# Kernel optimization log

Measured on AMD Instinct MI355X. Metric: run time of the kernel, lower is better.

## Reference

```python
import jax, jax.numpy as jnp
import numpy as np

N_NODES = 100000


def gcn_conv(x, src, dst, W, b, n_nodes):
    # PyG GCNConv: x' = D^{-1/2} (A + I) D^{-1/2} (x @ W) + b
    # src/dst already include self-loops.
    h = x @ W  # [N, out]
    deg = jax.ops.segment_sum(jnp.ones_like(src, dtype=x.dtype), dst,
                              num_segments=n_nodes)  # includes self-loops -> deg >= 1
    dinv = jax.lax.rsqrt(deg)
    norm = dinv[src] * dinv[dst]  # [E+N]
    msgs = h[src] * norm[:, None]  # [E+N, out]
    out = jax.ops.segment_sum(msgs, dst, num_segments=n_nodes)
    return out + b


def setup_inputs() -> dict:
    key = jax.random.key(0)
    k1, k2, k3, k4 = jax.random.split(key, 4)
    in_dim, hid_dim, out_dim = 64, 128, 64
    n_edges = 1_600_000
    x = jax.random.normal(k1, (N_NODES, in_dim), dtype=jnp.float32)
    edge_index = jax.random.randint(k2, (2, n_edges), 0, N_NODES, dtype=jnp.int64)
    # Glorot-ish init for weights
    W1 = jax.random.normal(k3, (in_dim, hid_dim), dtype=jnp.float32) * (1.0 / np.sqrt(in_dim))
    W2 = jax.random.normal(k4, (hid_dim, out_dim), dtype=jnp.float32) * (1.0 / np.sqrt(hid_dim))
    b1 = jnp.zeros((hid_dim,), dtype=jnp.float32)
    b2 = jnp.zeros((out_dim,), dtype=jnp.float32)
    return {"x": x, "edge_index": edge_index, "W1": W1, "b1": b1, "W2": W2, "b2": b2}


def reference(x, edge_index, W1, b1, W2, b2):
    n = x.shape[0]
    loops = jnp.arange(n, dtype=edge_index.dtype)
    src = jnp.concatenate([edge_index[0], loops])
    dst = jnp.concatenate([edge_index[1], loops])
    h = gcn_conv(x, src, dst, W1, b1, n)
    h = jax.nn.relu(h)
    out = gcn_conv(h, src, dst, W2, b2, n)
    return out
```

## Files before the change

kernel.cpp:

```cpp
#include <hip/hip_runtime.h>
#include <hip/hip_fp16.h>


#define DIM 64
#define NB 256
#define SPAN 391
#define BK_TILE 4096
#define BK_PER 16

typedef _Float16 f16x8 __attribute__((ext_vector_type(8)));
typedef float f32x4 __attribute__((ext_vector_type(4)));

__device__ __forceinline__ void atomAddF(float* p, float v) {
    unsafeAtomicAdd(p, v);
}

__device__ __forceinline__ void h8_add(const float4 v, float* acc) {
    const __half2* hp = (const __half2*)&v;
    #pragma unroll
    for (int i = 0; i < 4; ++i) {
        float2 t = __half22float2(hp[i]);
        acc[2 * i] += t.x;
        acc[2 * i + 1] += t.y;
    }
}
__device__ __forceinline__ float4 f8_to_h8(const float* f) {
    __half2 hh[4];
    hh[0] = __float22half2_rn(make_float2(f[0], f[1]));
    hh[1] = __float22half2_rn(make_float2(f[2], f[3]));
    hh[2] = __float22half2_rn(make_float2(f[4], f[5]));
    hh[3] = __float22half2_rn(make_float2(f[6], f[7]));
    return *(float4*)hh;
}

__device__ __forceinline__ void gather1(const float4* __restrict__ h4,
                                        const int* __restrict__ col,
                                        int e, int e1, int lane, float* accA, float* accB) {
    for (; e + 8 <= e1; e += 8) {
        int s0 = col[e], s1 = col[e + 1], s2 = col[e + 2], s3 = col[e + 3];
        int s4 = col[e + 4], s5 = col[e + 5], s6 = col[e + 6], s7 = col[e + 7];
        float4 v0 = h4[(long)s0 * 8 + lane];
        float4 v1 = h4[(long)s1 * 8 + lane];
        float4 v2 = h4[(long)s2 * 8 + lane];
        float4 v3 = h4[(long)s3 * 8 + lane];
        float4 v4 = h4[(long)s4 * 8 + lane];
        float4 v5 = h4[(long)s5 * 8 + lane];
        float4 v6 = h4[(long)s6 * 8 + lane];
        float4 v7 = h4[(long)s7 * 8 + lane];
        h8_add(v0, accA); h8_add(v1, accB);
        h8_add(v2, accA); h8_add(v3, accB);
        h8_add(v4, accA); h8_add(v5, accB);
        h8_add(v6, accA); h8_add(v7, accB);
    }
    for (; e + 2 <= e1; e += 2) {
        float4 v0 = h4[(long)col[e] * 8 + lane];
        float4 v1 = h4[(long)col[e + 1] * 8 + lane];
        h8_add(v0, accA); h8_add(v1, accB);
    }
    if (e < e1) h8_add(h4[(long)col[e] * 8 + lane], accA);
}

__global__ __launch_bounds__(256) void k_wconv(const float* __restrict__ W1,
                                               const float* __restrict__ W2,
                                               _Float16* __restrict__ W1t,
                                               _Float16* __restrict__ W2t,
                                               int* __restrict__ bcnt) {
    int idx = blockIdx.x * 256 + threadIdx.x;
    if (blockIdx.x == 0) bcnt[threadIdx.x] = 0;
    if (idx < 8192) {
        int n = idx >> 6, k = idx & 63;
        W1t[idx] = (_Float16)W1[k * 128 + n];
    } else if (idx < 16384) {
        int j = idx - 8192;
        int n = j >> 7, k = j & 127;
        W2t[j] = (_Float16)W2[k * 64 + n];
    }
}

__global__ __launch_bounds__(256) void k_hist256(const int* __restrict__ ei,
                                                 int* __restrict__ bucketCnt, int E) {
    __shared__ int h[NB];
    const int tid = threadIdx.x;
    h[tid] = 0;
    __syncthreads();
    const int base = blockIdx.x * BK_TILE;
    #pragma unroll
    for (int j = 0; j < BK_TILE; j += 256) {
        int e = base + j + tid;
        if (e < E) atomicAdd(&h[(unsigned)ei[E + e] / (unsigned)SPAN], 1);
    }
    __syncthreads();
    if (h[tid]) atomicAdd(&bucketCnt[tid], h[tid]);
}
__global__ __launch_bounds__(256) void k_scan_b(const int* __restrict__ bucketCnt,
                                                int* __restrict__ bucketBase,
                                                int* __restrict__ gcur) {
    __shared__ int s[NB];
    const int tid = threadIdx.x;
    int v = bucketCnt[tid];
    s[tid] = v;
    __syncthreads();
    for (int off = 1; off < NB; off <<= 1) {
        int t = (tid >= off) ? s[tid - off] : 0;
        __syncthreads();
        s[tid] += t;
        __syncthreads();
    }
    int ex = s[tid] - v;
    bucketBase[tid] = ex;
    gcur[tid] = ex;
    if (tid == NB - 1) bucketBase[NB] = s[NB - 1];
}

__global__ __launch_bounds__(256) void k_bucket(const int* __restrict__ ei,
                                                int* __restrict__ gcur,
                                                unsigned* __restrict__ pairs, int E) {
    __shared__ int scn[NB];
    __shared__ int run[NB];
    __shared__ int lbase[NB];
    __shared__ int gbase[NB];
    __shared__ unsigned stage[BK_TILE];
    __shared__ unsigned char bkt[BK_TILE];
    const int tid = threadIdx.x;
    const int base = blockIdx.x * BK_TILE;

    scn[tid] = 0;
    __syncthreads();

    unsigned pv[BK_PER];
    int bv[BK_PER];
    #pragma unroll
    for (int j = 0; j < BK_PER; ++j) {
        int e = base + j * 256 + tid;
        if (e < E) {
            unsigned s = (unsigned)ei[e];
            unsigned d = (unsigned)ei[E + e];
            int b = (int)(d / (unsigned)SPAN);
            bv[j] = b;
            pv[j] = (s << 9) | (d - (unsigned)b * SPAN);
            atomicAdd(&scn[b], 1);
        } else bv[j] = -1;
    }
    __syncthreads();
    int c = scn[tid];
    for (int off = 1; off < 256; off <<= 1) {
        int t = (tid >= off) ? scn[tid - off] : 0;
        __syncthreads();
        scn[tid] += t;
        __syncthreads();
    }
    int ex = scn[tid] - c;
    lbase[tid] = ex;
    run[tid] = ex;
    if (c > 0) gbase[tid] = atomicAdd(&gcur[tid], c);
    __syncthreads();

    #pragma unroll
    for (int j = 0; j < BK_PER; ++j) {
        if (bv[j] >= 0) {
            int p = atomicAdd(&run[bv[j]], 1);
            stage[p] = pv[j];
            bkt[p] = (unsigned char)bv[j];
        }
    }
    __syncthreads();

    int total = min(BK_TILE, E - base);
    for (int i = tid; i < total; i += 256) {
        int bb = bkt[i];
        pairs[gbase[bb] + (i - lbase[bb])] = stage[i];
    }
}

__global__ __launch_bounds__(256) void k_finish(const unsigned* __restrict__ pairs,
                                                const int* __restrict__ bucketBase,
                                                int* __restrict__ row_ptr,
                                                float* __restrict__ dinv,
                                                int* __restrict__ col,
                                                const float* __restrict__ x,
                                                __half* __restrict__ Y, int N) {
    __shared__ int lh[512];
    __shared__ int sa[512];
    __shared__ int sb[512];
    __shared__ int lcur[SPAN];
    const int tid = threadIdx.x;
    const int b = blockIdx.x;
    const int lo = b * SPAN;
    const int hi = min(lo + SPAN, N);
    const int nn = hi - lo;
    const int p0 = bucketBase[b];
    const int p1 = bucketBase[b + 1];

    for (int i = tid; i < 512; i += 256) lh[i] = 0;
    __syncthreads();
    for (int e = p0 + tid; e < p1; e += 256)
        atomicAdd(&lh[pairs[e] & 511u], 1);
    __syncthreads();
    int* cur = sa;
    int* nxt = sb;
    for (int i = tid; i < 512; i += 256) sa[i] = lh[i];
    __syncthreads();
    for (int off = 1; off < 512; off <<= 1) {
        for (int i = tid; i < 512; i += 256)
            nxt[i] = cur[i] + ((i >= off) ? cur[i - off] : 0);
        __syncthreads();
        int* t = cur; cur = nxt; nxt = t;
    }
    for (int i = tid; i < nn; i += 256) {
        int cnt  = lh[i];
        int base = p0 + cur[i] - cnt;
        row_ptr[lo + i] = base;
        lcur[i] = base;
        dinv[lo + i] = rsqrtf(1.0f + (float)cnt);
    }
    if (b == NB - 1 && tid == 0) row_ptr[N] = p1;
    __syncthreads();
    for (int e = p0 + tid; e < p1; e += 256) {
        unsigned pr = pairs[e];
        int pos = atomicAdd(&lcur[pr & 511u], 1);
        col[pos] = (int)(pr >> 9);
    }
    const int seg = tid & 7;
    for (int rr = tid >> 3; rr < nn; rr += 32) {
        float di = rsqrtf(1.0f + (float)lh[rr]);
        long row = lo + rr;
        float4 a = ((const float4*)x)[row * 16 + seg * 2];
        float4 c = ((const float4*)x)[row * 16 + seg * 2 + 1];
        float f[8] = {a.x * di, a.y * di, a.z * di, a.w * di,
                      c.x * di, c.y * di, c.z * di, c.w * di};
        ((float4*)Y)[row * 8 + seg] = f8_to_h8(f);
    }
}

__global__ __launch_bounds__(256) void k_agg_fin(const int* __restrict__ row_ptr,
                                                 const int* __restrict__ col,
                                                 const float* __restrict__ dinv,
                                                 const __half* __restrict__ ph,
                                                 const float* __restrict__ bias,
                                                 float* __restrict__ outv, int n) {
    int g = blockIdx.x * 32 + (threadIdx.x >> 3);
    if (g >= n) return;
    int lane = threadIdx.x & 7;
    const float4* h4 = (const float4*)ph;
    float accA[8] = {}, accB[8] = {};
    h8_add(h4[(long)g * 8 + lane], accA);
    gather1(h4, col, row_ptr[g], row_ptr[g + 1], lane, accA, accB);

    float di = dinv[g];
    float r[8];
    #pragma unroll
    for (int i = 0; i < 8; ++i) r[i] = (accA[i] + accB[i]) * di;
    float4 b0 = ((const float4*)bias)[lane * 2];
    float4 b1v = ((const float4*)bias)[lane * 2 + 1];
    r[0] += b0.x; r[1] += b0.y; r[2] += b0.z; r[3] += b0.w;
    r[4] += b1v.x; r[5] += b1v.y; r[6] += b1v.z; r[7] += b1v.w;
    *(float4*)&outv[(long)g * 64 + lane * 8]     = make_float4(r[0], r[1], r[2], r[3]);
    *(float4*)&outv[(long)g * 64 + lane * 8 + 4] = make_float4(r[4], r[5], r[6], r[7]);
}

__global__ __launch_bounds__(128) void k_agg_mlp(const int* __restrict__ row_ptr,
                                                 const int* __restrict__ col,
                                                 const float* __restrict__ dinv,
                                                 const __half* __restrict__ Y,
                                                 const _Float16* __restrict__ W1t,
                                                 const float* __restrict__ b1,
                                                 const _Float16* __restrict__ W2t,
                                                 _Float16* __restrict__ X,
                                                 int M) {
    __shared__ __align__(16) _Float16 Xs[32 * 72];
    __shared__ __align__(16) _Float16 Hs[32 * 136];
    const int tid = threadIdx.x;
    const int row0 = blockIdx.x * 32;
    const int grp = tid >> 3;
    const int lane = tid & 7;
    const float4* h4 = (const float4*)Y;

    #pragma unroll
    for (int hh = 0; hh < 2; ++hh) {
        const int lrow = grp + hh * 16;
        const int g = row0 + lrow;
        float r[8] = {};
        if (g < M) {
            float accA[8] = {}, accB[8] = {};
            h8_add(h4[(long)g * 8 + lane], accA);
            gather1(h4, col, row_ptr[g], row_ptr[g + 1], lane, accA, accB);
            float di = dinv[g];
            #pragma unroll
            for (int i = 0; i < 8; ++i) r[i] = (accA[i] + accB[i]) * di;
        }
        *(float4*)&Xs[lrow * 72 + lane * 8] = f8_to_h8(r);
    }
    __syncthreads();

    const int wv = tid >> 6;
    const int l64 = tid & 63;
    const int lr = l64 & 15;
    const int lg = l64 >> 4;

    f16x8 a0 = *(const f16x8*)&Xs[(wv * 16 + lr) * 72 + lg * 8];
    f16x8 a1 = *(const f16x8*)&Xs[(wv * 16 + lr) * 72 + 32 + lg * 8];
    const _Float16* wb1 = W1t + lr * 64 + lg * 8;
    f32x4 acc[8];
    #pragma unroll
    for (int nt = 0; nt < 8; ++nt) acc[nt] = (f32x4){0.f, 0.f, 0.f, 0.f};
    #pragma unroll
    for (int nt = 0; nt < 8; ++nt) {
        f16x8 b0 = *(const f16x8*)(wb1 + nt * 1024);
        f16x8 bK = *(const f16x8*)(wb1 + nt * 1024 + 32);
        acc[nt] = __builtin_amdgcn_mfma_f32_16x16x32_f16(a0, b0, acc[nt], 0, 0, 0);
        acc[nt] = __builtin_amdgcn_mfma_f32_16x16x32_f16(a1, bK, acc[nt], 0, 0, 0);
    }
    #pragma unroll
    for (int nt = 0; nt < 8; ++nt) {
        float bv = b1[nt * 16 + lr];
        #pragma unroll
        for (int r = 0; r < 4; ++r) {
            float h = fmaxf(acc[nt][r] + bv, 0.f);
            Hs[(wv * 16 + lg * 4 + r) * 136 + nt * 16 + lr] = (_Float16)h;
        }
    }
    __syncthreads();

    const _Float16* wb2 = W2t + lr * 128 + lg * 8;
    const _Float16* hrow = &Hs[(wv * 16 + lr) * 136 + lg * 8];
    f32x4 acc2[4];
    #pragma unroll
    for (int nt = 0; nt < 4; ++nt) acc2[nt] = (f32x4){0.f, 0.f, 0.f, 0.f};
    #pragma unroll
    for (int kk = 0; kk < 4; ++kk) {
        f16x8 a = *(const f16x8*)(hrow + kk * 32);
        #pragma unroll
        for (int nt = 0; nt < 4; ++nt) {
            f16x8 b = *(const f16x8*)(wb2 + nt * 2048 + kk * 32);
            acc2[nt] = __builtin_amdgcn_mfma_f32_16x16x32_f16(a, b, acc2[nt], 0, 0, 0);
        }
    }
    _Float16* Os = Xs;
    float sc[4];
    #pragma unroll
    for (int r = 0; r < 4; ++r) {
        int gr = row0 + wv * 16 + lg * 4 + r;
        sc[r] = (gr < M) ? dinv[gr] : 0.f;
    }
    #pragma unroll
    for (int nt = 0; nt < 4; ++nt) {
        #pragma unroll
        for (int r = 0; r < 4; ++r)
            Os[(wv * 16 + lg * 4 + r) * 72 + nt * 16 + lr] = (_Float16)(acc2[nt][r] * sc[r]);
    }
    __syncthreads();

    {
        int r = tid >> 2, c0 = (tid & 3) * 16;
        int gr = row0 + r;
        if (gr < M) {
            f16x8 v0 = *(const f16x8*)&Os[r * 72 + c0];
            f16x8 v1 = *(const f16x8*)&Os[r * 72 + c0 + 8];
            *(f16x8*)(X + (long)gr * 64 + c0) = v0;
            *(f16x8*)(X + (long)gr * 64 + c0 + 8) = v1;
        }
    }
}

__global__ __launch_bounds__(256) void k_init_deg(float* deg, int n) {
    int i = blockIdx.x * 256 + threadIdx.x;
    if (i < n) deg[i] = 1.0f;
}
__global__ __launch_bounds__(256) void k_count_deg(const int* __restrict__ ei, float* deg, int E) {
    int e = blockIdx.x * 256 + threadIdx.x;
    if (e < E) atomAddF(&deg[ei[E + e]], 1.0f);
}
__global__ __launch_bounds__(256) void k_rsqrt(float* deg, int n) {
    int i = blockIdx.x * 256 + threadIdx.x;
    if (i < n) deg[i] = rsqrtf(deg[i]);
}
template<bool BIAS>
__global__ __launch_bounds__(256) void k_self(const float* __restrict__ src,
                                              const float* __restrict__ dinv,
                                              const float* __restrict__ b,
                                              float* __restrict__ out, int n) {
    int g = blockIdx.x * 256 + threadIdx.x;
    int i = g >> 4, c = g & 15;
    if (i >= n) return;
    float di = dinv[i];
    float s = di * di;
    float4 v = *(const float4*)&src[(long)i * DIM + c * 4];
    float4 r = make_float4(v.x * s, v.y * s, v.z * s, v.w * s);
    if (BIAS) {
        float4 bv = *(const float4*)&b[c * 4];
        r.x += bv.x; r.y += bv.y; r.z += bv.z; r.w += bv.w;
    }
    *(float4*)&out[(long)i * DIM + c * 4] = r;
}
__global__ __launch_bounds__(256) void k_edge_agg(const int* __restrict__ ei,
                                                  const float* __restrict__ dinv,
                                                  const float* __restrict__ h,
                                                  float* __restrict__ out, int E) {
    int t = threadIdx.x;
    int e = blockIdx.x * 16 + (t >> 4);
    if (e >= E) return;
    int lane = t & 15;
    int s = ei[e];
    int d = ei[E + e];
    float norm = dinv[s] * dinv[d];
    float4 hv = *(const float4*)&h[(long)s * DIM + lane * 4];
    float* o = &out[(long)d * DIM + lane * 4];
    atomAddF(o + 0, hv.x * norm);
    atomAddF(o + 1, hv.y * norm);
    atomAddF(o + 2, hv.z * norm);
    atomAddF(o + 3, hv.w * norm);
}
__global__ __launch_bounds__(256) void k_mlp_f(const float* __restrict__ G,
                                               const float* __restrict__ W1,
                                               const float* __restrict__ b1,
                                               const float* __restrict__ W2,
                                               float* __restrict__ T, int M) {
    __shared__ float Ws[64 * 128];
    __shared__ float HA[64 * 132];
    const int tid = threadIdx.x;
    const int row0 = blockIdx.x * 64;
    const int ty = tid >> 4;
    const int tx = tid & 15;
    #pragma unroll
    for (int l = 0; l < 4; ++l) {
        int idx = l * 256 + tid;
        int r = idx >> 4, cv = idx & 15;
        int gr = row0 + r;
        float4 v = make_float4(0.f, 0.f, 0.f, 0.f);
        if (gr < M) v = *(const float4*)&G[(long)gr * DIM + cv * 4];
        *(float4*)&HA[r * 68 + cv * 4] = v;
    }
    #pragma unroll
    for (int l = 0; l < 8; ++l) {
        int idx = (l * 256 + tid) * 4;
        *(float4*)&Ws[idx] = *(const float4*)&W1[idx];
    }
    __syncthreads();
    float4 accA[4], accB[4];
    #pragma unroll
    for (int i = 0; i < 4; ++i) {
        accA[i] = make_float4(0.f, 0.f, 0.f, 0.f);
        accB[i] = make_float4(0.f, 0.f, 0.f, 0.f);
    }
    for (int k4 = 0; k4 < 64; k4 += 4) {
        float4 a[4];
        #pragma unroll
        for (int i = 0; i < 4; ++i) a[i] = *(const float4*)&HA[(ty * 4 + i) * 68 + k4];
        #pragma unroll
        for (int kk = 0; kk < 4; ++kk) {
            const float* wr = &Ws[(k4 + kk) * 128 + tx * 8];
            float4 wA = *(const float4*)wr;
            float4 wB = *(const float4*)(wr + 4);
            #pragma unroll
            for (int i = 0; i < 4; ++i) {
                float ak = (&a[i].x)[kk];
                accA[i].x += ak * wA.x; accA[i].y += ak * wA.y;
                accA[i].z += ak * wA.z; accA[i].w += ak * wA.w;
                accB[i].x += ak * wB.x; accB[i].y += ak * wB.y;
                accB[i].z += ak * wB.z; accB[i].w += ak * wB.w;
            }
        }
    }
    __syncthreads();
    {
        float4 bA = *(const float4*)&b1[tx * 8];
        float4 bB = *(const float4*)&b1[tx * 8 + 4];
        #pragma unroll
        for (int i = 0; i < 4; ++i) {
            float4 hA = make_float4(fmaxf(accA[i].x + bA.x, 0.f), fmaxf(accA[i].y + bA.y, 0.f),
                                    fmaxf(accA[i].z + bA.z, 0.f), fmaxf(accA[i].w + bA.w, 0.f));
            float4 hB = make_float4(fmaxf(accB[i].x + bB.x, 0.f), fmaxf(accB[i].y + bB.y, 0.f),
                                    fmaxf(accB[i].z + bB.z, 0.f), fmaxf(accB[i].w + bB.w, 0.f));
            *(float4*)&HA[(ty * 4 + i) * 132 + tx * 8 + 0] = hA;
            *(float4*)&HA[(ty * 4 + i) * 132 + tx * 8 + 4] = hB;
        }
    }
    #pragma unroll
    for (int l = 0; l < 8; ++l) {
        int idx = (l * 256 + tid) * 4;
        *(float4*)&Ws[idx] = *(const float4*)&W2[idx];
    }
    __syncthreads();
    float4 o[4];
    #pragma unroll
    for (int i = 0; i < 4; ++i) o[i] = make_float4(0.f, 0.f, 0.f, 0.f);
    for (int k4 = 0; k4 < 128; k4 += 4) {
        float4 a[4];
        #pragma unroll
        for (int i = 0; i < 4; ++i) a[i] = *(const float4*)&HA[(ty * 4 + i) * 132 + k4];
        #pragma unroll
        for (int kk = 0; kk < 4; ++kk) {
            float4 w = *(const float4*)&Ws[(k4 + kk) * 64 + tx * 4];
            #pragma unroll
            for (int i = 0; i < 4; ++i) {
                float ak = (&a[i].x)[kk];
                o[i].x += ak * w.x; o[i].y += ak * w.y;
                o[i].z += ak * w.z; o[i].w += ak * w.w;
            }
        }
    }
    #pragma unroll
    for (int i = 0; i < 4; ++i) {
        int gr = row0 + ty * 4 + i;
        if (gr < M) *(float4*)&T[(long)gr * DIM + tx * 4] = o[i];
    }
}

extern "C" void kernel_launch(void* const* d_in, const int* in_sizes, int n_in,
                              void* d_out, int out_size, void* d_ws, size_t ws_size,
                              hipStream_t stream) {
    const float* x  = (const float*)d_in[0];
    const int*   ei = (const int*)d_in[1];
    const float* W1 = (const float*)d_in[2];
    const float* b1 = (const float*)d_in[3];
    const float* W2 = (const float*)d_in[4];
    const float* b2 = (const float*)d_in[5];
    float* out = (float*)d_out;

    const int N = in_sizes[0] / DIM;
    const int E = in_sizes[1] / 2;

    const int gn   = (N + 255) / 256;
    const int ge   = (E + 255) / 256;
    const int gagg = (N + 31) / 32;
    const int gmlp = (N + 63) / 64;
    const int gbk  = (E + BK_TILE - 1) / BK_TILE;

    size_t off = 0;
    auto bump = [&](size_t bytes) { size_t o = off; off = (off + bytes + 255) & ~(size_t)255; return o; };
    size_t o_dinv   = bump((size_t)N * 4);
    size_t o_rowptr = bump((size_t)(N + 1) * 4);
    size_t o_bcnt   = bump(NB * 4);
    size_t o_bbase  = bump((NB + 1) * 4);
    size_t o_gcur   = bump(NB * 4);
    size_t o_col    = bump((size_t)E * 4);
    size_t o_X      = bump((size_t)N * DIM * 2);
    size_t o_Y      = bump((size_t)N * DIM * 2);
    size_t o_pairs  = bump((size_t)E * 4);
    size_t o_W1t    = bump(128 * 64 * 2);
    size_t o_W2t    = bump(64 * 128 * 2);
    size_t need_csr = off;

    char* ws = (char*)d_ws;

    if (ws_size >= need_csr) {
        float*    dinv   = (float*)(ws + o_dinv);
        int*      rowptr = (int*)(ws + o_rowptr);
        int*      bcnt   = (int*)(ws + o_bcnt);
        int*      bbase  = (int*)(ws + o_bbase);
        int*      gcur   = (int*)(ws + o_gcur);
        int*      col    = (int*)(ws + o_col);
        __half*   X      = (__half*)(ws + o_X);
        __half*   Y      = (__half*)(ws + o_Y);
        unsigned* pairs  = (unsigned*)(ws + o_pairs);
        _Float16* W1t    = (_Float16*)(ws + o_W1t);
        _Float16* W2t    = (_Float16*)(ws + o_W2t);

        k_wconv<<<64, 256, 0, stream>>>(W1, W2, W1t, W2t, bcnt);
        k_hist256<<<gbk, 256, 0, stream>>>(ei, bcnt, E);
        k_scan_b<<<1, 256, 0, stream>>>(bcnt, bbase, gcur);
        k_bucket<<<gbk, 256, 0, stream>>>(ei, gcur, pairs, E);
        k_finish<<<NB, 256, 0, stream>>>(pairs, bbase, rowptr, dinv, col, x, Y, N);
        k_agg_mlp<<<gagg, 128, 0, stream>>>(rowptr, col, dinv, Y, W1t, b1, W2t,
                                            (_Float16*)X, N);
        k_agg_fin<<<gagg, 256, 0, stream>>>(rowptr, col, dinv, X, b2, out, N);
    } else {
        float* dinv = (float*)ws;
        float* buf  = (float*)(ws + 512 * 1024);
        int grow16 = ((long)N * 16 + 255) / 256;
        int gedge = (E + 15) / 16;

        k_init_deg<<<gn, 256, 0, stream>>>(dinv, N);
        k_count_deg<<<ge, 256, 0, stream>>>(ei, dinv, E);
        k_rsqrt<<<gn, 256, 0, stream>>>(dinv, N);

        k_self<false><<<grow16, 256, 0, stream>>>(x, dinv, nullptr, buf, N);
        k_edge_agg<<<gedge, 256, 0, stream>>>(ei, dinv, x, buf, E);
        k_mlp_f<<<gmlp, 256, 0, stream>>>(buf, W1, b1, W2, buf, N);
        k_self<true><<<grow16, 256, 0, stream>>>(buf, dinv, b2, out, N);
        k_edge_agg<<<gedge, 256, 0, stream>>>(ei, dinv, buf, out, E);
    }
}
```

Measured before the change: 234.5 us.

## Split feature gathers into 16-column channel slabs for cache-resident aggregation

Measured after the change: 310.9 us. 1.33x slower.

```diff
diff --git a/kernel.cpp b/kernel.cpp
--- a/kernel.cpp
+++ b/kernel.cpp
@@ -33,31 +33,31 @@
     return *(float4*)hh;
 }
 
-__device__ __forceinline__ void gather1(const float4* __restrict__ h4,
+__device__ __forceinline__ void gatherc(const float4* __restrict__ P2,
                                         const int* __restrict__ col,
-                                        int e, int e1, int lane, float* accA, float* accB) {
+                                        int e, int e1, int p, float* accA, float* accB) {
     for (; e + 8 <= e1; e += 8) {
         int s0 = col[e], s1 = col[e + 1], s2 = col[e + 2], s3 = col[e + 3];
         int s4 = col[e + 4], s5 = col[e + 5], s6 = col[e + 6], s7 = col[e + 7];
-        float4 v0 = h4[(long)s0 * 8 + lane];
-        float4 v1 = h4[(long)s1 * 8 + lane];
-        float4 v2 = h4[(long)s2 * 8 + lane];
-        float4 v3 = h4[(long)s3 * 8 + lane];
-        float4 v4 = h4[(long)s4 * 8 + lane];
-        float4 v5 = h4[(long)s5 * 8 + lane];
-        float4 v6 = h4[(long)s6 * 8 + lane];
-        float4 v7 = h4[(long)s7 * 8 + lane];
+        float4 v0 = P2[(long)s0 * 2 + p];
+        float4 v1 = P2[(long)s1 * 2 + p];
+        float4 v2 = P2[(long)s2 * 2 + p];
+        float4 v3 = P2[(long)s3 * 2 + p];
+        float4 v4 = P2[(long)s4 * 2 + p];
+        float4 v5 = P2[(long)s5 * 2 + p];
+        float4 v6 = P2[(long)s6 * 2 + p];
+        float4 v7 = P2[(long)s7 * 2 + p];
         h8_add(v0, accA); h8_add(v1, accB);
         h8_add(v2, accA); h8_add(v3, accB);
         h8_add(v4, accA); h8_add(v5, accB);
         h8_add(v6, accA); h8_add(v7, accB);
     }
     for (; e + 2 <= e1; e += 2) {
-        float4 v0 = h4[(long)col[e] * 8 + lane];
-        float4 v1 = h4[(long)col[e + 1] * 8 + lane];
+        float4 v0 = P2[(long)col[e] * 2 + p];
+        float4 v1 = P2[(long)col[e + 1] * 2 + p];
         h8_add(v0, accA); h8_add(v1, accB);
     }
-    if (e < e1) h8_add(h4[(long)col[e] * 8 + lane], accA);
+    if (e < e1) h8_add(P2[(long)col[e] * 2 + p], accA);
 }
 
 __global__ __launch_bounds__(256) void k_wconv(const float* __restrict__ W1,
@@ -228,77 +228,66 @@
         float4 c = ((const float4*)x)[row * 16 + seg * 2 + 1];
         float f[8] = {a.x * di, a.y * di, a.z * di, a.w * di,
                       c.x * di, c.y * di, c.z * di, c.w * di};
-        ((float4*)Y)[row * 8 + seg] = f8_to_h8(f);
-    }
-}
-
-__global__ __launch_bounds__(256) void k_agg_fin(const int* __restrict__ row_ptr,
-                                                 const int* __restrict__ col,
-                                                 const float* __restrict__ dinv,
-                                                 const __half* __restrict__ ph,
-                                                 const float* __restrict__ bias,
-                                                 float* __restrict__ outv, int n) {
-    int g = blockIdx.x * 32 + (threadIdx.x >> 3);
+        __half* dst = Y + ((size_t)(seg >> 1) * N + row) * 16 + (seg & 1) * 8;
+        *(float4*)dst = f8_to_h8(f);
+    }
+}
+
+template<bool FINAL>
+__global__ __launch_bounds__(256) void k_aggc(const int* __restrict__ row_ptr,
+                                              const int* __restrict__ col,
+                                              const float* __restrict__ dinv,
+                                              const __half* __restrict__ slab,
+                                              const float* __restrict__ bias,
+                                              void* __restrict__ outv,
+                                              int c, int n) {
+    int g = blockIdx.x * 128 + (threadIdx.x >> 1);
     if (g >= n) return;
-    int lane = threadIdx.x & 7;
-    const float4* h4 = (const float4*)ph;
+    int p = threadIdx.x & 1;
+    const float4* P2 = (const float4*)slab;
     float accA[8] = {}, accB[8] = {};
-    h8_add(h4[(long)g * 8 + lane], accA);
-    gather1(h4, col, row_ptr[g], row_ptr[g + 1], lane, accA, accB);
+    h8_add(P2[(long)g * 2 + p], accA);
+    gatherc(P2, col, row_ptr[g], row_ptr[g + 1], p, accA, accB);
 
     float di = dinv[g];
     float r[8];
     #pragma unroll
     for (int i = 0; i < 8; ++i) r[i] = (accA[i] + accB[i]) * di;
-    float4 b0 = ((const float4*)bias)[lane * 2];
-    float4 b1v = ((const float4*)bias)[lane * 2 + 1];
-    r[0] += b0.x; r[1] += b0.y; r[2] += b0.z; r[3] += b0.w;
-    r[4] += b1v.x; r[5] += b1v.y; r[6] += b1v.z; r[7] += b1v.w;
-    *(float4*)&outv[(long)g * 64 + lane * 8]     = make_float4(r[0], r[1], r[2], r[3]);
-    *(float4*)&outv[(long)g * 64 + lane * 8 + 4] = make_float4(r[4], r[5], r[6], r[7]);
-}
-
-__global__ __launch_bounds__(128) void k_agg_mlp(const int* __restrict__ row_ptr,
-                                                 const int* __restrict__ col,
-                                                 const float* __restrict__ dinv,
-                                                 const __half* __restrict__ Y,
-                                                 const _Float16* __restrict__ W1t,
-                                                 const float* __restrict__ b1,
-                                                 const _Float16* __restrict__ W2t,
-                                                 _Float16* __restrict__ X,
-                                                 int M) {
-    __shared__ __align__(16) _Float16 Xs[32 * 72];
-    __shared__ __align__(16) _Float16 Hs[32 * 136];
+    if (FINAL) {
+        const float* bc = bias + c * 16 + p * 8;
+        #pragma unroll
+        for (int i = 0; i < 8; ++i) r[i] += bc[i];
+        float* o = (float*)outv + (long)g * 64 + c * 16 + p * 8;
+        *(float4*)o       = make_float4(r[0], r[1], r[2], r[3]);
+        *(float4*)(o + 4) = make_float4(r[4], r[5], r[6], r[7]);
+    } else {
+        __half* o = (__half*)outv + (long)g * 64 + c * 16 + p * 8;
+        *(float4*)o = f8_to_h8(r);
+    }
+}
+
+__global__ __launch_bounds__(256) void k_mlp_c(const _Float16* __restrict__ G,
+                                               const _Float16* __restrict__ W1t,
+                                               const float* __restrict__ b1,
+                                               const _Float16* __restrict__ W2t,
+                                               const float* __restrict__ dscale,
+                                               _Float16* __restrict__ Xch,
+                                               int M) {
+    __shared__ __align__(16) _Float16 Hs[64 * 136];
+    __shared__ __align__(16) _Float16 Os[64 * 72];
     const int tid = threadIdx.x;
-    const int row0 = blockIdx.x * 32;
-    const int grp = tid >> 3;
-    const int lane = tid & 7;
-    const float4* h4 = (const float4*)Y;
-
-    #pragma unroll
-    for (int hh = 0; hh < 2; ++hh) {
-        const int lrow = grp + hh * 16;
-        const int g = row0 + lrow;
-        float r[8] = {};
-        if (g < M) {
-            float accA[8] = {}, accB[8] = {};
-            h8_add(h4[(long)g * 8 + lane], accA);
-            gather1(h4, col, row_ptr[g], row_ptr[g + 1], lane, accA, accB);
-            float di = dinv[g];
-            #pragma unroll
-            for (int i = 0; i < 8; ++i) r[i] = (accA[i] + accB[i]) * di;
-        }
-        *(float4*)&Xs[lrow * 72 + lane * 8] = f8_to_h8(r);
-    }
-    __syncthreads();
-
+    const int row0 = blockIdx.x * 64;
     const int wv = tid >> 6;
     const int l64 = tid & 63;
     const int lr = l64 & 15;
     const int lg = l64 >> 4;
 
-    f16x8 a0 = *(const f16x8*)&Xs[(wv * 16 + lr) * 72 + lg * 8];
-    f16x8 a1 = *(const f16x8*)&Xs[(wv * 16 + lr) * 72 + 32 + lg * 8];
+    const int arow = row0 + wv * 16 + lr;
+    f16x8 a0 = {}, a1 = {};
+    if (arow < M) {
+        a0 = *(const f16x8*)(G + (long)arow * 64 + lg * 8);
+        a1 = *(const f16x8*)(G + (long)arow * 64 + 32 + lg * 8);
+    }
     const _Float16* wb1 = W1t + lr * 64 + lg * 8;
     f32x4 acc[8];
     #pragma unroll
@@ -335,12 +324,11 @@
             acc2[nt] = __builtin_amdgcn_mfma_f32_16x16x32_f16(a, b, acc2[nt], 0, 0, 0);
         }
     }
-    _Float16* Os = Xs;
     float sc[4];
     #pragma unroll
     for (int r = 0; r < 4; ++r) {
         int gr = row0 + wv * 16 + lg * 4 + r;
-        sc[r] = (gr < M) ? dinv[gr] : 0.f;
+        sc[r] = (gr < M) ? dscale[gr] : 0.f;
     }
     #pragma unroll
     for (int nt = 0; nt < 4; ++nt) {
@@ -356,8 +344,9 @@
         if (gr < M) {
             f16x8 v0 = *(const f16x8*)&Os[r * 72 + c0];
             f16x8 v1 = *(const f16x8*)&Os[r * 72 + c0 + 8];
-            *(f16x8*)(X + (long)gr * 64 + c0) = v0;
-            *(f16x8*)(X + (long)gr * 64 + c0 + 8) = v1;
+            _Float16* dst = Xch + ((size_t)(c0 >> 4) * M + gr) * 16;
+            *(f16x8*)dst = v0;
+            *(f16x8*)(dst + 8) = v1;
         }
     }
 }
@@ -522,7 +511,7 @@
 
     const int gn   = (N + 255) / 256;
     const int ge   = (E + 255) / 256;
-    const int gagg = (N + 31) / 32;
+    const int gac  = (N + 127) / 128;
     const int gmlp = (N + 63) / 64;
     const int gbk  = (E + BK_TILE - 1) / BK_TILE;
 
@@ -534,8 +523,9 @@
     size_t o_bbase  = bump((NB + 1) * 4);
     size_t o_gcur   = bump(NB * 4);
     size_t o_col    = bump((size_t)E * 4);
-    size_t o_X      = bump((size_t)N * DIM * 2);
     size_t o_Y      = bump((size_t)N * DIM * 2);
+    size_t o_Xf     = bump((size_t)N * DIM * 2);
+    size_t o_Xc     = bump((size_t)N * DIM * 2);
     size_t o_pairs  = bump((size_t)E * 4);
     size_t o_W1t    = bump(128 * 64 * 2);
     size_t o_W2t    = bump(64 * 128 * 2);
@@ -550,8 +540,9 @@
         int*      bbase  = (int*)(ws + o_bbase);
         int*      gcur   = (int*)(ws + o_gcur);
         int*      col    = (int*)(ws + o_col);
-        __half*   X      = (__half*)(ws + o_X);
         __half*   Y      = (__half*)(ws + o_Y);
+        __half*   Xf     = (__half*)(ws + o_Xf);
+        _Float16* Xc     = (_Float16*)(ws + o_Xc);
         unsigned* pairs  = (unsigned*)(ws + o_pairs);
         _Float16* W1t    = (_Float16*)(ws + o_W1t);
         _Float16* W2t    = (_Float16*)(ws + o_W2t);
@@ -561,9 +552,16 @@
         k_scan_b<<<1, 256, 0, stream>>>(bcnt, bbase, gcur);
         k_bucket<<<gbk, 256, 0, stream>>>(ei, gcur, pairs, E);
         k_finish<<<NB, 256, 0, stream>>>(pairs, bbase, rowptr, dinv, col, x, Y, N);
-        k_agg_mlp<<<gagg, 128, 0, stream>>>(rowptr, col, dinv, Y, W1t, b1, W2t,
-                                            (_Float16*)X, N);
-        k_agg_fin<<<gagg, 256, 0, stream>>>(rowptr, col, dinv, X, b2, out, N);
+        for (int c = 0; c < 4; ++c)
+            k_aggc<false><<<gac, 256, 0, stream>>>(
+                rowptr, col, dinv, (const __half*)(Y + (size_t)c * N * 16),
+                nullptr, (void*)Xf, c, N);
+        k_mlp_c<<<gmlp, 256, 0, stream>>>((const _Float16*)Xf, W1t, b1, W2t, dinv,
+                                          Xc, N);
+        for (int c = 0; c < 4; ++c)
+            k_aggc<true><<<gac, 256, 0, stream>>>(
+                rowptr, col, dinv, (const __half*)(Xc + (size_t)c * N * 16),
+                b2, (void*)out, c, N);
     } else {
         float* dinv = (float*)ws;
         float* buf  = (float*)(ws + 512 * 1024);
```
